# Performance work log

Hardware: AMD Instinct MI355X
Metric: run time of the kernel (lower is better)

## Reference

```python
import jax, jax.numpy as jnp
import numpy as np

H, L, C, B = 128, 32, 32, 1


def _grid_sample_3d(feat, grid):
    """Trilinear grid_sample, align_corners=True, zeros padding.

    feat: [B, C, D, H, W]; grid: [B, P, 3] in [-1, 1].
    Torch convention: grid channel 0 indexes W, 1 indexes H, 2 indexes D.
    Returns [B, C, P].
    """
    Bb, Cc, D, Hh, W = feat.shape
    ix = (grid[..., 0] + 1.0) * 0.5 * (W - 1)
    iy = (grid[..., 1] + 1.0) * 0.5 * (Hh - 1)
    iz = (grid[..., 2] + 1.0) * 0.5 * (D - 1)
    x0 = jnp.floor(ix); y0 = jnp.floor(iy); z0 = jnp.floor(iz)
    # interpolation weights, broadcast over channel dim -> [B, 1, P]
    wx = (ix - x0)[:, None, :]; wy = (iy - y0)[:, None, :]; wz = (iz - z0)[:, None, :]
    x0i = jnp.clip(x0.astype(jnp.int32), 0, W - 1)
    y0i = jnp.clip(y0.astype(jnp.int32), 0, Hh - 1)
    z0i = jnp.clip(z0.astype(jnp.int32), 0, D - 1)
    x1i = jnp.clip(x0i + 1, 0, W - 1)
    y1i = jnp.clip(y0i + 1, 0, Hh - 1)
    z1i = jnp.clip(z0i + 1, 0, D - 1)

    def gather(f, z, y, x):  # f: [C,D,H,W]; idx: [P] -> [C,P]
        return f[:, z, y, x]

    g = jax.vmap(gather)
    c = lambda z, y, x: g(feat, z, y, x)  # [B,C,P]
    out = (c(z0i, y0i, x0i) * (1 - wz) * (1 - wy) * (1 - wx)
         + c(z0i, y0i, x1i) * (1 - wz) * (1 - wy) * wx
         + c(z0i, y1i, x0i) * (1 - wz) * wy * (1 - wx)
         + c(z0i, y1i, x1i) * (1 - wz) * wy * wx
         + c(z1i, y0i, x0i) * wz * (1 - wy) * (1 - wx)
         + c(z1i, y0i, x1i) * wz * (1 - wy) * wx
         + c(z1i, y1i, x0i) * wz * wy * (1 - wx)
         + c(z1i, y1i, x1i) * wz * wy * wx)
    return out


def _normalize(verts):
    # verts: [B, X, Y, Z, 3] -> normalized grid [B, P, 3] in [-1, 1]
    b = verts.reshape(verts.shape[0], -1, 3)
    mn = jnp.min(b, axis=1, keepdims=True)
    mx = jnp.max(b, axis=1, keepdims=True)
    return jax.lax.stop_gradient((b - mn) / (mx - mn) * 2.0 - 1.0)


def setup_inputs() -> dict:
    key = jax.random.key(0)
    ks = jax.random.split(key, 6)
    return {
        "feat0": jax.random.normal(ks[0], (B, C, H, H, L), dtype=jnp.float32),
        "feat1": jax.random.normal(ks[1], (B, C, H, L, H), dtype=jnp.float32),
        "feat2": jax.random.normal(ks[2], (B, C, L, H, H), dtype=jnp.float32),
        "verts0": jax.random.uniform(ks[3], (B, H, H, L, 3), dtype=jnp.float32),
        "verts1": jax.random.uniform(ks[4], (B, H, L, H, 3), dtype=jnp.float32),
        "verts2": jax.random.uniform(ks[5], (B, L, H, H, 3), dtype=jnp.float32),
    }


def reference(feat0, feat1, feat2, verts0, verts1, verts2):
    feats = [feat0, feat1, feat2]
    grids = [_normalize(v) for v in (verts0, verts1, verts2)]  # each [B,P,3]
    outs = []
    for i in range(3):
        out = feats[i]
        for j in range(3):
            if i == j:
                continue
            sampled = _grid_sample_3d(feats[j], grids[i])  # [B,C,P]
            out = out + sampled.reshape(feats[i].shape)  # communication_type='sum'
        outs.append(out)
    # stack flattened per-grid outputs (all share numel X*Y*Z)
    return jnp.stack([o.reshape(o.shape[0], o.shape[1], -1) for o in outs])  # [3,B,C,P]
```

## Files before the change

### kernel.cpp

```cpp
#include <hip/hip_runtime.h>
#include <hip/hip_fp16.h>


#define WS_P 524288
#define NCH 32
#define NBIN 512
#define NBLK 256
#define PPB  2048
#define BP   64
#define NSB  (WS_P / BP)

__device__ __forceinline__ float ntloadf(const float* p) {
    return __builtin_nontemporal_load(p);
}
__device__ __forceinline__ void ntstoref(float* p, float v) {
    __builtin_nontemporal_store(v, p);
}

__device__ __forceinline__ unsigned encf(float f) {
    unsigned b = __float_as_uint(f);
    return (b & 0x80000000u) ? ~b : (b | 0x80000000u);
}
__device__ __forceinline__ float decf(unsigned u) {
    unsigned b = (u & 0x80000000u) ? (u & 0x7FFFFFFFu) : ~u;
    return __uint_as_float(b);
}

__device__ __forceinline__ int bin_of(float u) {
    int b = (int)(u * 8.0f);
    return b < 0 ? 0 : (b > 7 ? 7 : b);
}

__global__ void init_mm_kernel(unsigned* mm) {
    int t = threadIdx.x;
    if (t < 18) mm[t] = (t & 1) ? 0u : 0xFFFFFFFFu;
}

__global__ __launch_bounds__(256) void minmax_kernel(
    const float* __restrict__ v0, const float* __restrict__ v1,
    const float* __restrict__ v2, unsigned* __restrict__ mm)
{
    const int g = blockIdx.y;
    const float* v = (g == 0) ? v0 : (g == 1) ? v1 : v2;
    const int tid = threadIdx.x;

    float mn[3] = { INFINITY, INFINITY, INFINITY };
    float mx[3] = { -INFINITY, -INFINITY, -INFINITY };

    for (int idx = blockIdx.x * 256 + tid; idx < WS_P; idx += 128 * 256) {
        #pragma unroll
        for (int k = 0; k < 3; k++) {
            float f = v[(size_t)idx * 3 + k];
            mn[k] = fminf(mn[k], f);
            mx[k] = fmaxf(mx[k], f);
        }
    }

    __shared__ float smn[3][256];
    __shared__ float smx[3][256];
    #pragma unroll
    for (int k = 0; k < 3; k++) { smn[k][tid] = mn[k]; smx[k][tid] = mx[k]; }
    __syncthreads();

    for (int s = 128; s > 0; s >>= 1) {
        if (tid < s) {
            #pragma unroll
            for (int k = 0; k < 3; k++) {
                smn[k][tid] = fminf(smn[k][tid], smn[k][tid + s]);
                smx[k][tid] = fmaxf(smx[k][tid], smx[k][tid + s]);
            }
        }
        __syncthreads();
    }

    if (tid == 0) {
        #pragma unroll
        for (int k = 0; k < 3; k++) {
            atomicMin(&mm[g * 6 + k * 2 + 0], encf(smn[k][0]));
            atomicMax(&mm[g * 6 + k * 2 + 1], encf(smx[k][0]));
        }
    }
}

__global__ __launch_bounds__(256) void block_hist_kernel(
    const float* __restrict__ v0, const float* __restrict__ v1,
    const float* __restrict__ v2, const unsigned* __restrict__ mm,
    unsigned* __restrict__ counts)
{
    const int g = blockIdx.y;
    const int blk = blockIdx.x;
    const float* v = (g == 0) ? v0 : (g == 1) ? v1 : v2;
    const int tid = threadIdx.x;

    __shared__ unsigned h[NBIN];
    for (int i = tid; i < NBIN; i += 256) h[i] = 0u;
    __syncthreads();

    float mn[3], inv_r[3];
    #pragma unroll
    for (int k = 0; k < 3; k++) {
        mn[k] = decf(mm[g * 6 + k * 2 + 0]);
        inv_r[k] = 1.0f / (decf(mm[g * 6 + k * 2 + 1]) - mn[k]);
    }

    #pragma unroll
    for (int r = 0; r < PPB / 256; r++) {
        int p = blk * PPB + r * 256 + tid;
        float u0 = (v[(size_t)p * 3 + 0] - mn[0]) * inv_r[0];
        float u1 = (v[(size_t)p * 3 + 1] - mn[1]) * inv_r[1];
        float u2 = (v[(size_t)p * 3 + 2] - mn[2]) * inv_r[2];
        int key = (bin_of(u2) * 8 + bin_of(u1)) * 8 + bin_of(u0);
        atomicAdd(&h[key], 1u);
    }
    __syncthreads();
    for (int i = tid; i < NBIN; i += 256)
        counts[((size_t)g * NBIN + i) * NBLK + blk] = h[i];
}

__global__ __launch_bounds__(256) void scanA_kernel(
    unsigned* __restrict__ counts, unsigned* __restrict__ tot)
{
    const int bin = blockIdx.x;
    const int g = blockIdx.y;
    const int t = threadIdx.x;
    size_t rowo = ((size_t)g * NBIN + bin) * NBLK;

    unsigned v = counts[rowo + t];
    __shared__ unsigned s[NBLK];
    s[t] = v;
    __syncthreads();
    for (int off = 1; off < NBLK; off <<= 1) {
        unsigned x = (t >= off) ? s[t - off] : 0u;
        __syncthreads();
        s[t] += x;
        __syncthreads();
    }
    counts[rowo + t] = s[t] - v;
    if (t == NBLK - 1) tot[g * NBIN + bin] = s[t];
}

__global__ void scanB_kernel(const unsigned* __restrict__ tot,
                             unsigned* __restrict__ binbase)
{
    const int g = blockIdx.x;
    const int t = threadIdx.x;
    unsigned v = tot[g * NBIN + t];
    __shared__ unsigned s[NBIN];
    s[t] = v;
    __syncthreads();
    for (int off = 1; off < NBIN; off <<= 1) {
        unsigned x = (t >= off) ? s[t - off] : 0u;
        __syncthreads();
        s[t] += x;
        __syncthreads();
    }
    binbase[g * NBIN + t] = s[t] - v;
}

__global__ __launch_bounds__(256) void scatter_kernel(
    const float* __restrict__ v0, const float* __restrict__ v1,
    const float* __restrict__ v2, const unsigned* __restrict__ mm,
    const unsigned* __restrict__ bscan, const unsigned* __restrict__ binbase,
    uint4* __restrict__ rec)
{
    const int g = blockIdx.y;
    const int blk = blockIdx.x;
    const float* v = (g == 0) ? v0 : (g == 1) ? v1 : v2;
    const int tid = threadIdx.x;

    __shared__ unsigned h[NBIN];
    for (int i = tid; i < NBIN; i += 256)
        h[i] = binbase[g * NBIN + i] + bscan[((size_t)g * NBIN + i) * NBLK + blk];
    __syncthreads();

    float mn[3], inv_r[3];
    #pragma unroll
    for (int k = 0; k < 3; k++) {
        mn[k] = decf(mm[g * 6 + k * 2 + 0]);
        inv_r[k] = 1.0f / (decf(mm[g * 6 + k * 2 + 1]) - mn[k]);
    }

    #pragma unroll
    for (int r = 0; r < PPB / 256; r++) {
        int p = blk * PPB + r * 256 + tid;
        float u0 = (v[(size_t)p * 3 + 0] - mn[0]) * inv_r[0];
        float u1 = (v[(size_t)p * 3 + 1] - mn[1]) * inv_r[1];
        float u2 = (v[(size_t)p * 3 + 2] - mn[2]) * inv_r[2];
        int key = (bin_of(u2) * 8 + bin_of(u1)) * 8 + bin_of(u0);
        unsigned pos = atomicAdd(&h[key], 1u);
        rec[(size_t)g * WS_P + pos] =
            make_uint4(__float_as_uint(u0 * 2.0f - 1.0f),
                       __float_as_uint(u1 * 2.0f - 1.0f),
                       __float_as_uint(u2 * 2.0f - 1.0f), (unsigned)p);
    }
}

__global__ __launch_bounds__(256) void transpose16_kernel(
    const float* __restrict__ f0, const float* __restrict__ f1,
    const float* __restrict__ f2,
    __half* __restrict__ t0, __half* __restrict__ t1, __half* __restrict__ t2)
{
    const int j = blockIdx.y;
    const float* in = (j == 0) ? f0 : (j == 1) ? f1 : f2;
    __half* out = (j == 0) ? t0 : (j == 1) ? t1 : t2;

    __shared__ float tile[32][33];
    const int tx = threadIdx.x;
    const int ty = threadIdx.y;
    const int n0 = blockIdx.x * 32;

    #pragma unroll
    for (int r = 0; r < 4; r++) {
        int c = ty + r * 8;
        tile[c][tx] = ntloadf(&in[(size_t)c * WS_P + n0 + tx]);
    }
    __syncthreads();

    __half2* out2 = reinterpret_cast<__half2*>(out);
    const int tid = ty * 32 + tx;
    const int cp = tid & 15;
    #pragma unroll
    for (int r = 0; r < 2; r++) {
        int pl = (tid >> 4) + r * 16;
        float a = tile[cp * 2 + 0][pl];
        float b = tile[cp * 2 + 1][pl];
        out2[(size_t)(n0 + pl) * 16 + cp] = __floats2half2_rn(a, b);
    }
}

template<int I>
__device__ __forceinline__ void sample_sorted_body(
    const __half* __restrict__ t0, const __half* __restrict__ t1,
    const __half* __restrict__ t2, const uint4* __restrict__ rec,
    __half* __restrict__ temps, uint2 (*ow)[17], unsigned* pp)
{
    constexpr int Dd[3] = { 128, 128, 32 };
    constexpr int Hh[3] = { 128, 32, 128 };
    constexpr int Ww[3] = { 32, 128, 128 };

    const int bid = blockIdx.x;
    const int swz = (bid & 7) * (NSB / 8) + (bid >> 3);
    const int tid = threadIdx.x;
    const int slot0 = swz * BP;

    if (tid < BP) {
        uint4 r = rec[(size_t)I * WS_P + slot0 + tid];
        float g0 = __uint_as_float(r.x);
        float g1 = __uint_as_float(r.y);
        float g2 = __uint_as_float(r.z);
        pp[tid] = r.w;
        #pragma unroll
        for (int jj = 0; jj < 2; jj++) {
            const int j = (I + 1 + jj) % 3;
            const int W = Ww[j], H = Hh[j], D = Dd[j];

            float ix = (g0 + 1.0f) * 0.5f * (float)(W - 1);
            float iy = (g1 + 1.0f) * 0.5f * (float)(H - 1);
            float iz = (g2 + 1.0f) * 0.5f * (float)(D - 1);
            float fx = floorf(ix), fy = floorf(iy), fz = floorf(iz);
            float wx = ix - fx, wy = iy - fy, wz = iz - fz;

            int x0 = (int)fx; x0 = x0 < 0 ? 0 : (x0 > W - 1 ? W - 1 : x0);
            int y0 = (int)fy; y0 = y0 < 0 ? 0 : (y0 > H - 1 ? H - 1 : y0);
            int z0 = (int)fz; z0 = z0 < 0 ? 0 : (z0 > D - 1 ? D - 1 : z0);
            int x1 = (x0 + 1 > W - 1) ? W - 1 : x0 + 1;
            int y1 = (y0 + 1 > H - 1) ? H - 1 : y0 + 1;
            int z1 = (z0 + 1 > D - 1) ? D - 1 : z0 + 1;

            float ux = 1.0f - wx, uy = 1.0f - wy, uz = 1.0f - wz;
            float w[8] = { uz * uy * ux, uz * uy * wx, uz * wy * ux, uz * wy * wx,
                           wz * uy * ux, wz * uy * wx, wz * wy * ux, wz * wy * wx };

            int r00 = (z0 * H + y0) * W;
            int r01 = (z0 * H + y1) * W;
            int r10 = (z1 * H + y0) * W;
            int r11 = (z1 * H + y1) * W;
            int o[8] = { r00 + x0, r00 + x1, r01 + x0, r01 + x1,
                         r10 + x0, r10 + x1, r11 + x0, r11 + x1 };

            #pragma unroll
            for (int hh = 0; hh < 8; hh++)
                ow[tid][jj * 8 + hh] =
                    make_uint2((unsigned)o[hh] * 64u, __float_as_uint(w[hh]));
        }
    }
    __syncthreads();

    const int q = tid >> 2;
    const int l = tid & 3;
    const char* sA = (const char*)((I == 0) ? t1 : (I == 1) ? t2 : t0);
    const char* sB = (const char*)((I == 0) ? t2 : (I == 1) ? t0 : t1);

    float a0 = 0.f, a1 = 0.f, a2 = 0.f, a3 = 0.f;
    float a4 = 0.f, a5 = 0.f, a6 = 0.f, a7 = 0.f;

    #pragma unroll
    for (int cn = 0; cn < 16; cn++) {
        uint2 e = ow[q][cn];
        const char* base = (cn < 8) ? sA : sB;
        uint4 d = *reinterpret_cast<const uint4*>(base + e.x + (unsigned)l * 16u);
        float w = __uint_as_float(e.y);
        float2 f0 = __half22float2(*reinterpret_cast<__half2*>(&d.x));
        float2 f1 = __half22float2(*reinterpret_cast<__half2*>(&d.y));
        float2 f2 = __half22float2(*reinterpret_cast<__half2*>(&d.z));
        float2 f3 = __half22float2(*reinterpret_cast<__half2*>(&d.w));
        a0 = fmaf(w, f0.x, a0); a1 = fmaf(w, f0.y, a1);
        a2 = fmaf(w, f1.x, a2); a3 = fmaf(w, f1.y, a3);
        a4 = fmaf(w, f2.x, a4); a5 = fmaf(w, f2.y, a5);
        a6 = fmaf(w, f3.x, a6); a7 = fmaf(w, f3.y, a7);
    }

    __half2 h0 = __floats2half2_rn(a0, a1);
    __half2 h1 = __floats2half2_rn(a2, a3);
    __half2 h2 = __floats2half2_rn(a4, a5);
    __half2 h3 = __floats2half2_rn(a6, a7);
    uint4 wv;
    wv.x = *reinterpret_cast<unsigned*>(&h0);
    wv.y = *reinterpret_cast<unsigned*>(&h1);
    wv.z = *reinterpret_cast<unsigned*>(&h2);
    wv.w = *reinterpret_cast<unsigned*>(&h3);

    unsigned p = pp[q];
    char* dst = (char*)(temps + (size_t)I * NCH * WS_P) + (size_t)p * 64u;
    reinterpret_cast<uint4*>(dst)[l] = wv;
}

__global__ __launch_bounds__(256, 8) void sample_all_kernel(
    const __half* __restrict__ t0, const __half* __restrict__ t1,
    const __half* __restrict__ t2, const uint4* __restrict__ rec,
    __half* __restrict__ temps)
{
    __shared__ uint2 ow[BP][17];
    __shared__ unsigned pp[BP];
    switch (blockIdx.y) {
        case 0: sample_sorted_body<0>(t0, t1, t2, rec, temps, ow, pp); break;
        case 1: sample_sorted_body<1>(t0, t1, t2, rec, temps, ow, pp); break;
        default: sample_sorted_body<2>(t0, t1, t2, rec, temps, ow, pp); break;
    }
}

__global__ __launch_bounds__(256, 8) void finish_kernel(
    const __half* __restrict__ temps,
    const __half* __restrict__ t0, const __half* __restrict__ t1,
    const __half* __restrict__ t2, float* __restrict__ out)
{
    __shared__ float sb[32][33];
    const int I = blockIdx.y;
    const __half* ti = (I == 0) ? t0 : (I == 1) ? t1 : t2;
    const int tid = threadIdx.x;
    const int p0 = blockIdx.x * 32;
    const int lpt = tid >> 3;
    const int subp = tid & 7;
    const int p = p0 + lpt;

    const uint2* tI = reinterpret_cast<const uint2*>(temps + (size_t)I * NCH * WS_P);
    uint2 tv = tI[(size_t)p * 8 + subp];
    float2 s0 = __half22float2(*reinterpret_cast<__half2*>(&tv.x));
    float2 s1 = __half22float2(*reinterpret_cast<__half2*>(&tv.y));
    uint2 rI = reinterpret_cast<const uint2*>(ti)[(size_t)p * 8 + subp];
    float2 i0 = __half22float2(*reinterpret_cast<__half2*>(&rI.x));
    float2 i1 = __half22float2(*reinterpret_cast<__half2*>(&rI.y));

    sb[lpt][subp * 4 + 0] = s0.x + i0.x;
    sb[lpt][subp * 4 + 1] = s0.y + i0.y;
    sb[lpt][subp * 4 + 2] = s1.x + i1.x;
    sb[lpt][subp * 4 + 3] = s1.y + i1.y;
    __syncthreads();

    float* op = out + (size_t)I * NCH * WS_P;
    #pragma unroll
    for (int it = 0; it < 4; it++) {
        int c = it * 8 + (tid >> 5);
        size_t off = (size_t)c * WS_P + p0 + (tid & 31);
        ntstoref(&op[off], sb[tid & 31][c]);
    }
}

template<int I>
__device__ __forceinline__ float4 gather2(
    const __half* __restrict__ t0, const __half* __restrict__ t1,
    const __half* __restrict__ t2, float g0, float g1, float g2, int subp)
{
    constexpr int Dd[3] = { 128, 128, 32 };
    constexpr int Hh[3] = { 128, 32, 128 };
    constexpr int Ww[3] = { 32, 128, 128 };

    float4 acc = make_float4(0.f, 0.f, 0.f, 0.f);
    #pragma unroll
    for (int jj = 0; jj < 2; jj++) {
        const int j = (I + 1 + jj) % 3;
        const __half* src = (j == 0) ? t0 : (j == 1) ? t1 : t2;
        const int W = Ww[j], H = Hh[j], D = Dd[j];

        float ix = (g0 + 1.0f) * 0.5f * (float)(W - 1);
        float iy = (g1 + 1.0f) * 0.5f * (float)(H - 1);
        float iz = (g2 + 1.0f) * 0.5f * (float)(D - 1);
        float fx = floorf(ix), fy = floorf(iy), fz = floorf(iz);
        float wx = ix - fx, wy = iy - fy, wz = iz - fz;

        int x0 = (int)fx; x0 = x0 < 0 ? 0 : (x0 > W - 1 ? W - 1 : x0);
        int y0 = (int)fy; y0 = y0 < 0 ? 0 : (y0 > H - 1 ? H - 1 : y0);
        int z0 = (int)fz; z0 = z0 < 0 ? 0 : (z0 > D - 1 ? D - 1 : z0);
        int x1 = (x0 + 1 > W - 1) ? W - 1 : x0 + 1;
        int y1 = (y0 + 1 > H - 1) ? H - 1 : y0 + 1;
        int z1 = (z0 + 1 > D - 1) ? D - 1 : z0 + 1;

        float ux = 1.0f - wx, uy = 1.0f - wy, uz = 1.0f - wz;
        float w[8] = { uz * uy * ux, uz * uy * wx, uz * wy * ux, uz * wy * wx,
                       wz * uy * ux, wz * uy * wx, wz * wy * ux, wz * wy * wx };

        int r00 = (z0 * H + y0) * W;
        int r01 = (z0 * H + y1) * W;
        int r10 = (z1 * H + y0) * W;
        int r11 = (z1 * H + y1) * W;
        int o[8] = { r00 + x0, r00 + x1, r01 + x0, r01 + x1,
                     r10 + x0, r10 + x1, r11 + x0, r11 + x1 };

        const uint2* s8 = reinterpret_cast<const uint2*>(src);
        #pragma unroll
        for (int h = 0; h < 2; h++) {
            uint2 rA = s8[(size_t)o[h * 4 + 0] * 8 + subp];
            uint2 rB = s8[(size_t)o[h * 4 + 1] * 8 + subp];
            uint2 rC = s8[(size_t)o[h * 4 + 2] * 8 + subp];
            uint2 rD = s8[(size_t)o[h * 4 + 3] * 8 + subp];
            float wA = w[h * 4 + 0], wB = w[h * 4 + 1];
            float wC = w[h * 4 + 2], wD = w[h * 4 + 3];
            float2 a0 = __half22float2(*reinterpret_cast<__half2*>(&rA.x));
            float2 a1 = __half22float2(*reinterpret_cast<__half2*>(&rA.y));
            float2 b0 = __half22float2(*reinterpret_cast<__half2*>(&rB.x));
            float2 b1 = __half22float2(*reinterpret_cast<__half2*>(&rB.y));
            float2 c0 = __half22float2(*reinterpret_cast<__half2*>(&rC.x));
            float2 c1 = __half22float2(*reinterpret_cast<__half2*>(&rC.y));
            float2 d0 = __half22float2(*reinterpret_cast<__half2*>(&rD.x));
            float2 d1 = __half22float2(*reinterpret_cast<__half2*>(&rD.y));
            acc.x = fmaf(wA, a0.x, acc.x); acc.y = fmaf(wA, a0.y, acc.y);
            acc.z = fmaf(wA, a1.x, acc.z); acc.w = fmaf(wA, a1.y, acc.w);
            acc.x = fmaf(wB, b0.x, acc.x); acc.y = fmaf(wB, b0.y, acc.y);
            acc.z = fmaf(wB, b1.x, acc.z); acc.w = fmaf(wB, b1.y, acc.w);
            acc.x = fmaf(wC, c0.x, acc.x); acc.y = fmaf(wC, c0.y, acc.y);
            acc.z = fmaf(wC, c1.x, acc.z); acc.w = fmaf(wC, c1.y, acc.w);
            acc.x = fmaf(wD, d0.x, acc.x); acc.y = fmaf(wD, d0.y, acc.y);
            acc.z = fmaf(wD, d1.x, acc.z); acc.w = fmaf(wD, d1.y, acc.w);
        }
    }
    return acc;
}

template<int I>
__device__ __forceinline__ void sample_body(
    const __half* __restrict__ t0, const __half* __restrict__ t1,
    const __half* __restrict__ t2,
    const float* __restrict__ v0, const float* __restrict__ v1,
    const float* __restrict__ v2,
    const unsigned* __restrict__ mm, float* __restrict__ out,
    float (*sb)[33])
{
    const int tid = threadIdx.x;
    const int p = blockIdx.x * 32 + (tid >> 3);
    const int subp = tid & 7;

    const float* verts = (I == 0) ? v0 : (I == 1) ? v1 : v2;
    const __half* ti   = (I == 0) ? t0 : (I == 1) ? t1 : t2;

    float g[3];
    #pragma unroll
    for (int k = 0; k < 3; k++) {
        float mn = decf(mm[I * 6 + k * 2 + 0]);
        float mx = decf(mm[I * 6 + k * 2 + 1]);
        float vv = ntloadf(&verts[(size_t)p * 3 + k]);
        g[k] = (vv - mn) / (mx - mn) * 2.0f - 1.0f;
    }

    float4 acc = gather2<I>(t0, t1, t2, g[0], g[1], g[2], subp);
    {
        uint2 rI = reinterpret_cast<const uint2*>(ti)[(size_t)p * 8 + subp];
        float2 i0 = __half22float2(*reinterpret_cast<__half2*>(&rI.x));
        float2 i1 = __half22float2(*reinterpret_cast<__half2*>(&rI.y));
        acc.x += i0.x; acc.y += i0.y; acc.z += i1.x; acc.w += i1.y;
    }

    const int pl = tid >> 3;
    sb[pl][subp * 4 + 0] = acc.x;
    sb[pl][subp * 4 + 1] = acc.y;
    sb[pl][subp * 4 + 2] = acc.z;
    sb[pl][subp * 4 + 3] = acc.w;
    __syncthreads();

    const int p0 = blockIdx.x * 32;
    float* op = out + (size_t)I * NCH * WS_P;
    #pragma unroll
    for (int it = 0; it < 4; it++) {
        int c = it * 8 + (tid >> 5);
        size_t off = (size_t)c * WS_P + p0 + (tid & 31);
        ntstoref(&op[off], sb[tid & 31][c]);
    }
}

__global__ __launch_bounds__(256, 8) void fused_sample_kernel(
    const __half* __restrict__ t0, const __half* __restrict__ t1,
    const __half* __restrict__ t2,
    const float* __restrict__ v0, const float* __restrict__ v1,
    const float* __restrict__ v2,
    const unsigned* __restrict__ mm, float* __restrict__ out)
{
    __shared__ float sb[32][33];
    switch (blockIdx.y) {
        case 0: sample_body<0>(t0, t1, t2, v0, v1, v2, mm, out, sb); break;
        case 1: sample_body<1>(t0, t1, t2, v0, v1, v2, mm, out, sb); break;
        default: sample_body<2>(t0, t1, t2, v0, v1, v2, mm, out, sb); break;
    }
}

template<int I>
__global__ __launch_bounds__(256) void sample_fallback_kernel(
    const float* __restrict__ f0, const float* __restrict__ f1,
    const float* __restrict__ f2,
    const float* __restrict__ v0, const float* __restrict__ v1,
    const float* __restrict__ v2,
    const unsigned* __restrict__ mm, float* __restrict__ out)
{
    constexpr int Dd[3] = { 128, 128, 32 };
    constexpr int Hh[3] = { 128, 32, 128 };
    constexpr int Ww[3] = { 32, 128, 128 };

    const int p = blockIdx.x * 256 + threadIdx.x;
    const float* verts = (I == 0) ? v0 : (I == 1) ? v1 : v2;
    const float* fi    = (I == 0) ? f0 : (I == 1) ? f1 : f2;

    float g[3];
    #pragma unroll
    for (int k = 0; k < 3; k++) {
        float mn = decf(mm[I * 6 + k * 2 + 0]);
        float mx = decf(mm[I * 6 + k * 2 + 1]);
        float vv = verts[(size_t)p * 3 + k];
        g[k] = (vv - mn) / (mx - mn) * 2.0f - 1.0f;
    }

    float acc[NCH];
    #pragma unroll
    for (int c = 0; c < NCH; c++) acc[c] = fi[(size_t)c * WS_P + p];

    #pragma unroll
    for (int jj = 0; jj < 2; jj++) {
        const int j = (I + 1 + jj) % 3;
        const float* src = (j == 0) ? f0 : (j == 1) ? f1 : f2;
        const int W = Ww[j], H = Hh[j], D = Dd[j];

        float ix = (g[0] + 1.0f) * 0.5f * (float)(W - 1);
        float iy = (g[1] + 1.0f) * 0.5f * (float)(H - 1);
        float iz = (g[2] + 1.0f) * 0.5f * (float)(D - 1);
        float fx = floorf(ix), fy = floorf(iy), fz = floorf(iz);
        float wx = ix - fx, wy = iy - fy, wz = iz - fz;

        int x0 = (int)fx; x0 = x0 < 0 ? 0 : (x0 > W - 1 ? W - 1 : x0);
        int y0 = (int)fy; y0 = y0 < 0 ? 0 : (y0 > H - 1 ? H - 1 : y0);
        int z0 = (int)fz; z0 = z0 < 0 ? 0 : (z0 > D - 1 ? D - 1 : z0);
        int x1 = (x0 + 1 > W - 1) ? W - 1 : x0 + 1;
        int y1 = (y0 + 1 > H - 1) ? H - 1 : y0 + 1;
        int z1 = (z0 + 1 > D - 1) ? D - 1 : z0 + 1;

        float ux = 1.0f - wx, uy = 1.0f - wy, uz = 1.0f - wz;
        float w[8] = { uz * uy * ux, uz * uy * wx, uz * wy * ux, uz * wy * wx,
                       wz * uy * ux, wz * uy * wx, wz * wy * ux, wz * wy * wx };

        int r00 = (z0 * H + y0) * W;
        int r01 = (z0 * H + y1) * W;
        int r10 = (z1 * H + y0) * W;
        int r11 = (z1 * H + y1) * W;
        int o[8] = { r00 + x0, r00 + x1, r01 + x0, r01 + x1,
                     r10 + x0, r10 + x1, r11 + x0, r11 + x1 };

        #pragma unroll
        for (int cn = 0; cn < 8; cn++) {
            float wt = w[cn];
            const float* sp = src + o[cn];
            #pragma unroll
            for (int c = 0; c < NCH; c++)
                acc[c] = fmaf(wt, sp[(size_t)c * WS_P], acc[c]);
        }
    }

    float* op = out + (size_t)I * NCH * WS_P + p;
    #pragma unroll
    for (int c = 0; c < NCH; c++) op[(size_t)c * WS_P] = acc[c];
}

extern "C" void kernel_launch(void* const* d_in, const int* in_sizes, int n_in,
                              void* d_out, int out_size, void* d_ws, size_t ws_size,
                              hipStream_t stream) {
    const float* f0 = (const float*)d_in[0];
    const float* f1 = (const float*)d_in[1];
    const float* f2 = (const float*)d_in[2];
    const float* v0 = (const float*)d_in[3];
    const float* v1 = (const float*)d_in[4];
    const float* v2 = (const float*)d_in[5];
    float* out = (float*)d_out;

    char* ws = (char*)d_ws;
    const size_t FEAT_ELEMS = (size_t)NCH * WS_P;
    const size_t MB = 1u << 20;
    unsigned* mm = (unsigned*)ws;
    unsigned* tot = (unsigned*)(ws + 4096);
    unsigned* binbase = (unsigned*)(ws + 16384);
    __half* t0 = (__half*)(ws + MB);
    __half* t1 = t0 + FEAT_ELEMS;
    __half* t2 = t1 + FEAT_ELEMS;
    size_t off = MB + 3 * FEAT_ELEMS * sizeof(__half);
    uint4* rec = (uint4*)(ws + off);       off += 3 * (size_t)WS_P * 16;
    unsigned* counts = (unsigned*)(ws + off);
    off += (size_t)3 * NBLK * NBIN * 4;
    __half* temps = (__half*)(ws + off);
    off += 3 * FEAT_ELEMS * sizeof(__half);
    const size_t FULL_NEED = off;
    const size_t MID_NEED = MB + 3 * FEAT_ELEMS * sizeof(__half);

    hipLaunchKernelGGL(init_mm_kernel, dim3(1), dim3(32), 0, stream, mm);
    hipLaunchKernelGGL(minmax_kernel, dim3(128, 3), dim3(256), 0, stream,
                       v0, v1, v2, mm);

    if (ws_size >= FULL_NEED) {
        hipLaunchKernelGGL(block_hist_kernel, dim3(NBLK, 3), dim3(256), 0, stream,
                           v0, v1, v2, mm, counts);
        hipLaunchKernelGGL(scanA_kernel, dim3(NBIN, 3), dim3(NBLK), 0, stream,
                           counts, tot);
        hipLaunchKernelGGL(scanB_kernel, dim3(3), dim3(NBIN), 0, stream,
                           tot, binbase);
        hipLaunchKernelGGL(scatter_kernel, dim3(NBLK, 3), dim3(256), 0, stream,
                           v0, v1, v2, mm, counts, binbase, rec);
        hipLaunchKernelGGL(transpose16_kernel, dim3(WS_P / 32, 3), dim3(32, 8), 0,
                           stream, f0, f1, f2, t0, t1, t2);
        hipLaunchKernelGGL(sample_all_kernel, dim3(NSB, 3), dim3(256), 0,
                           stream, t0, t1, t2, rec, temps);
        hipLaunchKernelGGL(finish_kernel, dim3(WS_P / 32, 3), dim3(256), 0,
                           stream, temps, t0, t1, t2, out);
    } else if (ws_size >= MID_NEED) {
        hipLaunchKernelGGL(transpose16_kernel, dim3(WS_P / 32, 3), dim3(32, 8), 0,
                           stream, f0, f1, f2, t0, t1, t2);
        hipLaunchKernelGGL(fused_sample_kernel, dim3(WS_P / 32, 3), dim3(256), 0,
                           stream, t0, t1, t2, v0, v1, v2, mm, out);
    } else {
        hipLaunchKernelGGL((sample_fallback_kernel<0>), dim3(WS_P / 256), dim3(256), 0,
                           stream, f0, f1, f2, v0, v1, v2, mm, out);
        hipLaunchKernelGGL((sample_fallback_kernel<1>), dim3(WS_P / 256), dim3(256), 0,
                           stream, f0, f1, f2, v0, v1, v2, mm, out);
        hipLaunchKernelGGL((sample_fallback_kernel<2>), dim3(WS_P / 256), dim3(256), 0,
                           stream, f0, f1, f2, v0, v1, v2, mm, out);
    }
}
```

Before: 330.6 us.

## Fuse transpose into histogram kernel, parallelize setup, use half2 FMA accumulation

Merges the feature transpose into the histogram kernel as extra blocks, so one launch covers both and the transpose overlaps the histogram work. In the sorted sampler, the per-point offset/weight setup is now split across all 256 threads (4 per point, each doing 4 corners) rather than 64 threads doing 16 corners each. The inner gather loop now accumulates with packed half2 FMAs instead of converting to float, which cuts ALU work but lowers accumulation precision to fp16. The 1D-block transpose kernel is kept only for the mid-workspace path.

```diff
diff --git a/kernel.cpp b/kernel.cpp
--- a/kernel.cpp
+++ b/kernel.cpp
@@ -9,6 +9,7 @@
 #define PPB  2048
 #define BP   64
 #define NSB  (WS_P / BP)
+#define NTB  (WS_P / 32)
 
 __device__ __forceinline__ float ntloadf(const float* p) {
     return __builtin_nontemporal_load(p);
@@ -82,39 +83,68 @@
     }
 }
 
-__global__ __launch_bounds__(256) void block_hist_kernel(
+__global__ __launch_bounds__(256) void transpose_hist_kernel(
+    const float* __restrict__ f0, const float* __restrict__ f1,
+    const float* __restrict__ f2,
+    __half* __restrict__ t0, __half* __restrict__ t1, __half* __restrict__ t2,
     const float* __restrict__ v0, const float* __restrict__ v1,
     const float* __restrict__ v2, const unsigned* __restrict__ mm,
     unsigned* __restrict__ counts)
 {
+    __shared__ float tile[32][33];
+    __shared__ unsigned h[NBIN];
     const int g = blockIdx.y;
-    const int blk = blockIdx.x;
-    const float* v = (g == 0) ? v0 : (g == 1) ? v1 : v2;
     const int tid = threadIdx.x;
 
-    __shared__ unsigned h[NBIN];
-    for (int i = tid; i < NBIN; i += 256) h[i] = 0u;
-    __syncthreads();
-
-    float mn[3], inv_r[3];
-    #pragma unroll
-    for (int k = 0; k < 3; k++) {
-        mn[k] = decf(mm[g * 6 + k * 2 + 0]);
-        inv_r[k] = 1.0f / (decf(mm[g * 6 + k * 2 + 1]) - mn[k]);
-    }
-
-    #pragma unroll
-    for (int r = 0; r < PPB / 256; r++) {
-        int p = blk * PPB + r * 256 + tid;
-        float u0 = (v[(size_t)p * 3 + 0] - mn[0]) * inv_r[0];
-        float u1 = (v[(size_t)p * 3 + 1] - mn[1]) * inv_r[1];
-        float u2 = (v[(size_t)p * 3 + 2] - mn[2]) * inv_r[2];
-        int key = (bin_of(u2) * 8 + bin_of(u1)) * 8 + bin_of(u0);
-        atomicAdd(&h[key], 1u);
-    }
-    __syncthreads();
-    for (int i = tid; i < NBIN; i += 256)
-        counts[((size_t)g * NBIN + i) * NBLK + blk] = h[i];
+    if (blockIdx.x < NBLK) {
+        const int blk = blockIdx.x;
+        const float* v = (g == 0) ? v0 : (g == 1) ? v1 : v2;
+        for (int i = tid; i < NBIN; i += 256) h[i] = 0u;
+        __syncthreads();
+
+        float mn[3], inv_r[3];
+        #pragma unroll
+        for (int k = 0; k < 3; k++) {
+            mn[k] = decf(mm[g * 6 + k * 2 + 0]);
+            inv_r[k] = 1.0f / (decf(mm[g * 6 + k * 2 + 1]) - mn[k]);
+        }
+        #pragma unroll
+        for (int r = 0; r < PPB / 256; r++) {
+            int p = blk * PPB + r * 256 + tid;
+            float u0 = (v[(size_t)p * 3 + 0] - mn[0]) * inv_r[0];
+            float u1 = (v[(size_t)p * 3 + 1] - mn[1]) * inv_r[1];
+            float u2 = (v[(size_t)p * 3 + 2] - mn[2]) * inv_r[2];
+            int key = (bin_of(u2) * 8 + bin_of(u1)) * 8 + bin_of(u0);
+            atomicAdd(&h[key], 1u);
+        }
+        __syncthreads();
+        for (int i = tid; i < NBIN; i += 256)
+            counts[((size_t)g * NBIN + i) * NBLK + blk] = h[i];
+    } else {
+        const int bt = blockIdx.x - NBLK;
+        const float* in = (g == 0) ? f0 : (g == 1) ? f1 : f2;
+        __half* out = (g == 0) ? t0 : (g == 1) ? t1 : t2;
+        const int tx = tid & 31;
+        const int ty = tid >> 5;
+        const int n0 = bt * 32;
+
+        #pragma unroll
+        for (int r = 0; r < 4; r++) {
+            int c = ty + r * 8;
+            tile[c][tx] = ntloadf(&in[(size_t)c * WS_P + n0 + tx]);
+        }
+        __syncthreads();
+
+        __half2* out2 = reinterpret_cast<__half2*>(out);
+        const int cp = tid & 15;
+        #pragma unroll
+        for (int r = 0; r < 2; r++) {
+            int pl = (tid >> 4) + r * 16;
+            float a = tile[cp * 2 + 0][pl];
+            float b = tile[cp * 2 + 1][pl];
+            out2[(size_t)(n0 + pl) * 16 + cp] = __floats2half2_rn(a, b);
+        }
+    }
 }
 
 __global__ __launch_bounds__(256) void scanA_kernel(
@@ -195,39 +225,6 @@
     }
 }
 
-__global__ __launch_bounds__(256) void transpose16_kernel(
-    const float* __restrict__ f0, const float* __restrict__ f1,
-    const float* __restrict__ f2,
-    __half* __restrict__ t0, __half* __restrict__ t1, __half* __restrict__ t2)
-{
-    const int j = blockIdx.y;
-    const float* in = (j == 0) ? f0 : (j == 1) ? f1 : f2;
-    __half* out = (j == 0) ? t0 : (j == 1) ? t1 : t2;
-
-    __shared__ float tile[32][33];
-    const int tx = threadIdx.x;
-    const int ty = threadIdx.y;
-    const int n0 = blockIdx.x * 32;
-
-    #pragma unroll
-    for (int r = 0; r < 4; r++) {
-        int c = ty + r * 8;
-        tile[c][tx] = ntloadf(&in[(size_t)c * WS_P + n0 + tx]);
-    }
-    __syncthreads();
-
-    __half2* out2 = reinterpret_cast<__half2*>(out);
-    const int tid = ty * 32 + tx;
-    const int cp = tid & 15;
-    #pragma unroll
-    for (int r = 0; r < 2; r++) {
-        int pl = (tid >> 4) + r * 16;
-        float a = tile[cp * 2 + 0][pl];
-        float b = tile[cp * 2 + 1][pl];
-        out2[(size_t)(n0 + pl) * 16 + cp] = __floats2half2_rn(a, b);
-    }
-}
-
 template<int I>
 __device__ __forceinline__ void sample_sorted_body(
     const __half* __restrict__ t0, const __half* __restrict__ t1,
@@ -242,83 +239,78 @@
     const int swz = (bid & 7) * (NSB / 8) + (bid >> 3);
     const int tid = threadIdx.x;
     const int slot0 = swz * BP;
-
-    if (tid < BP) {
-        uint4 r = rec[(size_t)I * WS_P + slot0 + tid];
+    const int q = tid >> 2;
+    const int l = tid & 3;
+
+    {
+        uint4 r = rec[(size_t)I * WS_P + slot0 + q];
+        if (l == 0) pp[q] = r.w;
         float g0 = __uint_as_float(r.x);
         float g1 = __uint_as_float(r.y);
         float g2 = __uint_as_float(r.z);
-        pp[tid] = r.w;
-        #pragma unroll
-        for (int jj = 0; jj < 2; jj++) {
-            const int j = (I + 1 + jj) % 3;
-            const int W = Ww[j], H = Hh[j], D = Dd[j];
-
-            float ix = (g0 + 1.0f) * 0.5f * (float)(W - 1);
-            float iy = (g1 + 1.0f) * 0.5f * (float)(H - 1);
-            float iz = (g2 + 1.0f) * 0.5f * (float)(D - 1);
-            float fx = floorf(ix), fy = floorf(iy), fz = floorf(iz);
-            float wx = ix - fx, wy = iy - fy, wz = iz - fz;
-
-            int x0 = (int)fx; x0 = x0 < 0 ? 0 : (x0 > W - 1 ? W - 1 : x0);
-            int y0 = (int)fy; y0 = y0 < 0 ? 0 : (y0 > H - 1 ? H - 1 : y0);
-            int z0 = (int)fz; z0 = z0 < 0 ? 0 : (z0 > D - 1 ? D - 1 : z0);
-            int x1 = (x0 + 1 > W - 1) ? W - 1 : x0 + 1;
-            int y1 = (y0 + 1 > H - 1) ? H - 1 : y0 + 1;
-            int z1 = (z0 + 1 > D - 1) ? D - 1 : z0 + 1;
-
-            float ux = 1.0f - wx, uy = 1.0f - wy, uz = 1.0f - wz;
-            float w[8] = { uz * uy * ux, uz * uy * wx, uz * wy * ux, uz * wy * wx,
-                           wz * uy * ux, wz * uy * wx, wz * wy * ux, wz * wy * wx };
-
-            int r00 = (z0 * H + y0) * W;
-            int r01 = (z0 * H + y1) * W;
-            int r10 = (z1 * H + y0) * W;
-            int r11 = (z1 * H + y1) * W;
-            int o[8] = { r00 + x0, r00 + x1, r01 + x0, r01 + x1,
-                         r10 + x0, r10 + x1, r11 + x0, r11 + x1 };
-
-            #pragma unroll
-            for (int hh = 0; hh < 8; hh++)
-                ow[tid][jj * 8 + hh] =
-                    make_uint2((unsigned)o[hh] * 64u, __float_as_uint(w[hh]));
-        }
-    }
-    __syncthreads();
-
-    const int q = tid >> 2;
-    const int l = tid & 3;
+
+        const int jj = l >> 1;
+        const int j = (I + 1 + jj) % 3;
+        const int W = Ww[j], H = Hh[j], D = Dd[j];
+
+        float ix = (g0 + 1.0f) * 0.5f * (float)(W - 1);
+        float iy = (g1 + 1.0f) * 0.5f * (float)(H - 1);
+        float iz = (g2 + 1.0f) * 0.5f * (float)(D - 1);
+        float fx = floorf(ix), fy = floorf(iy), fz = floorf(iz);
+        float wx = ix - fx, wy = iy - fy, wz = iz - fz;
+
+        int x0 = (int)fx; x0 = x0 < 0 ? 0 : (x0 > W - 1 ? W - 1 : x0);
+        int y0 = (int)fy; y0 = y0 < 0 ? 0 : (y0 > H - 1 ? H - 1 : y0);
+        int z0 = (int)fz; z0 = z0 < 0 ? 0 : (z0 > D - 1 ? D - 1 : z0);
+        int x1 = (x0 + 1 > W - 1) ? W - 1 : x0 + 1;
+        int y1 = (y0 + 1 > H - 1) ? H - 1 : y0 + 1;
+        int z1 = (z0 + 1 > D - 1) ? D - 1 : z0 + 1;
+
+        float ux = 1.0f - wx, uy = 1.0f - wy, uz = 1.0f - wz;
+
+        const int b = l & 1;
+        int zz = b ? z1 : z0;
+        float fzw = b ? wz : uz;
+        int rb0 = (zz * H + y0) * W;
+        int rb1 = (zz * H + y1) * W;
+        unsigned o4[4] = { (unsigned)(rb0 + x0), (unsigned)(rb0 + x1),
+                           (unsigned)(rb1 + x0), (unsigned)(rb1 + x1) };
+        float w4[4] = { fzw * uy * ux, fzw * uy * wx,
+                        fzw * wy * ux, fzw * wy * wx };
+
+        const int basei = jj * 8 + b * 4;
+        #pragma unroll
+        for (int c = 0; c < 4; c++) {
+            __half2 ww = __floats2half2_rn(w4[c], w4[c]);
+            ow[q][basei + c] =
+                make_uint2(o4[c] * 64u, *reinterpret_cast<unsigned*>(&ww));
+        }
+    }
+    __syncthreads();
+
     const char* sA = (const char*)((I == 0) ? t1 : (I == 1) ? t2 : t0);
     const char* sB = (const char*)((I == 0) ? t2 : (I == 1) ? t0 : t1);
 
-    float a0 = 0.f, a1 = 0.f, a2 = 0.f, a3 = 0.f;
-    float a4 = 0.f, a5 = 0.f, a6 = 0.f, a7 = 0.f;
+    __half2 acc0 = __floats2half2_rn(0.f, 0.f);
+    __half2 acc1 = acc0, acc2 = acc0, acc3 = acc0;
 
     #pragma unroll
     for (int cn = 0; cn < 16; cn++) {
         uint2 e = ow[q][cn];
         const char* base = (cn < 8) ? sA : sB;
         uint4 d = *reinterpret_cast<const uint4*>(base + e.x + (unsigned)l * 16u);
-        float w = __uint_as_float(e.y);
-        float2 f0 = __half22float2(*reinterpret_cast<__half2*>(&d.x));
-        float2 f1 = __half22float2(*reinterpret_cast<__half2*>(&d.y));
-        float2 f2 = __half22float2(*reinterpret_cast<__half2*>(&d.z));
-        float2 f3 = __half22float2(*reinterpret_cast<__half2*>(&d.w));
-        a0 = fmaf(w, f0.x, a0); a1 = fmaf(w, f0.y, a1);
-        a2 = fmaf(w, f1.x, a2); a3 = fmaf(w, f1.y, a3);
-        a4 = fmaf(w, f2.x, a4); a5 = fmaf(w, f2.y, a5);
-        a6 = fmaf(w, f3.x, a6); a7 = fmaf(w, f3.y, a7);
-    }
-
-    __half2 h0 = __floats2half2_rn(a0, a1);
-    __half2 h1 = __floats2half2_rn(a2, a3);
-    __half2 h2 = __floats2half2_rn(a4, a5);
-    __half2 h3 = __floats2half2_rn(a6, a7);
+        __half2 ww = *reinterpret_cast<__half2*>(&e.y);
+        acc0 = __hfma2(*reinterpret_cast<__half2*>(&d.x), ww, acc0);
+        acc1 = __hfma2(*reinterpret_cast<__half2*>(&d.y), ww, acc1);
+        acc2 = __hfma2(*reinterpret_cast<__half2*>(&d.z), ww, acc2);
+        acc3 = __hfma2(*reinterpret_cast<__half2*>(&d.w), ww, acc3);
+    }
+
     uint4 wv;
-    wv.x = *reinterpret_cast<unsigned*>(&h0);
-    wv.y = *reinterpret_cast<unsigned*>(&h1);
-    wv.z = *reinterpret_cast<unsigned*>(&h2);
-    wv.w = *reinterpret_cast<unsigned*>(&h3);
+    wv.x = *reinterpret_cast<unsigned*>(&acc0);
+    wv.y = *reinterpret_cast<unsigned*>(&acc1);
+    wv.z = *reinterpret_cast<unsigned*>(&acc2);
+    wv.w = *reinterpret_cast<unsigned*>(&acc3);
 
     unsigned p = pp[q];
     char* dst = (char*)(temps + (size_t)I * NCH * WS_P) + (size_t)p * 64u;
@@ -511,6 +503,39 @@
     }
 }
 
+__global__ __launch_bounds__(256) void transpose16_kernel(
+    const float* __restrict__ f0, const float* __restrict__ f1,
+    const float* __restrict__ f2,
+    __half* __restrict__ t0, __half* __restrict__ t1, __half* __restrict__ t2)
+{
+    const int j = blockIdx.y;
+    const float* in = (j == 0) ? f0 : (j == 1) ? f1 : f2;
+    __half* out = (j == 0) ? t0 : (j == 1) ? t1 : t2;
+
+    __shared__ float tile[32][33];
+    const int tid = threadIdx.x;
+    const int tx = tid & 31;
+    const int ty = tid >> 5;
+    const int n0 = blockIdx.x * 32;
+
+    #pragma unroll
+    for (int r = 0; r < 4; r++) {
+        int c = ty + r * 8;
+        tile[c][tx] = ntloadf(&in[(size_t)c * WS_P + n0 + tx]);
+    }
+    __syncthreads();
+
+    __half2* out2 = reinterpret_cast<__half2*>(out);
+    const int cp = tid & 15;
+    #pragma unroll
+    for (int r = 0; r < 2; r++) {
+        int pl = (tid >> 4) + r * 16;
+        float a = tile[cp * 2 + 0][pl];
+        float b = tile[cp * 2 + 1][pl];
+        out2[(size_t)(n0 + pl) * 16 + cp] = __floats2half2_rn(a, b);
+    }
+}
+
 template<int I>
 __global__ __launch_bounds__(256) void sample_fallback_kernel(
     const float* __restrict__ f0, const float* __restrict__ f1,
@@ -619,7 +644,8 @@
                        v0, v1, v2, mm);
 
     if (ws_size >= FULL_NEED) {
-        hipLaunchKernelGGL(block_hist_kernel, dim3(NBLK, 3), dim3(256), 0, stream,
+        hipLaunchKernelGGL(transpose_hist_kernel, dim3(NBLK + NTB, 3), dim3(256),
+                           0, stream, f0, f1, f2, t0, t1, t2,
                            v0, v1, v2, mm, counts);
         hipLaunchKernelGGL(scanA_kernel, dim3(NBIN, 3), dim3(NBLK), 0, stream,
                            counts, tot);
@@ -627,14 +653,12 @@
                            tot, binbase);
         hipLaunchKernelGGL(scatter_kernel, dim3(NBLK, 3), dim3(256), 0, stream,
                            v0, v1, v2, mm, counts, binbase, rec);
-        hipLaunchKernelGGL(transpose16_kernel, dim3(WS_P / 32, 3), dim3(32, 8), 0,
-                           stream, f0, f1, f2, t0, t1, t2);
         hipLaunchKernelGGL(sample_all_kernel, dim3(NSB, 3), dim3(256), 0,
                            stream, t0, t1, t2, rec, temps);
         hipLaunchKernelGGL(finish_kernel, dim3(WS_P / 32, 3), dim3(256), 0,
                            stream, temps, t0, t1, t2, out);
     } else if (ws_size >= MID_NEED) {
-        hipLaunchKernelGGL(transpose16_kernel, dim3(WS_P / 32, 3), dim3(32, 8), 0,
+        hipLaunchKernelGGL(transpose16_kernel, dim3(NTB, 3), dim3(256), 0,
                            stream, f0, f1, f2, t0, t1, t2);
         hipLaunchKernelGGL(fused_sample_kernel, dim3(WS_P / 32, 3), dim3(256), 0,
                            stream, t0, t1, t2, v0, v1, v2, mm, out);
```

After: 286.5 us. 1.15x faster.
